# Kernel tuning notes

Hardware: AMD Instinct MI355X
Metric: run time of the kernel (lower is better)

## Reference

```python
import jax, jax.numpy as jnp
import numpy as np

B = 32           # graphs in batch
N_PER = 512      # nodes per graph
N = B * N_PER    # 16384 total nodes (block-diagonal batched graph)
E = N * 16       # 262144 edges
D_IN = 128
D_OUT = 128
ASSIGN = 2048    # total clusters = B * K
K = ASSIGN // B  # 64 clusters per graph


def setup_inputs() -> dict:
    key = jax.random.key(0)
    ks = jax.random.split(key, 6)
    h = jax.random.normal(ks[0], (N, D_IN), jnp.float32)
    # edges confined within each graph -> block-diagonal batched adjacency
    gid = jnp.repeat(jnp.arange(B), E // B)
    edge_src = (jax.random.randint(ks[1], (E,), 0, N_PER) + gid * N_PER).astype(jnp.int32)
    edge_dst = (jax.random.randint(ks[2], (E,), 0, N_PER) + gid * N_PER).astype(jnp.int32)
    # GraphSage NodeApply linears: Linear(2*in, out)
    stdv_f = 1.0 / np.sqrt(2 * D_IN)
    W_feat = jax.random.uniform(ks[3], (2 * D_IN, D_OUT), jnp.float32, -stdv_f, stdv_f)
    b_feat = jnp.zeros((D_OUT,), jnp.float32)
    W_pool = jax.random.uniform(ks[4], (2 * D_IN, ASSIGN), jnp.float32, -stdv_f, stdv_f)
    b_pool = jnp.zeros((ASSIGN,), jnp.float32)
    return {"h": h, "W_feat": W_feat, "b_feat": b_feat,
            "W_pool": W_pool, "b_pool": b_pool,
            "edge_src": edge_src, "edge_dst": edge_dst}


def _graphsage(h, W, b, src, dst):
    # mean aggregation over in-neighbors (dropout=0, batch_norm off)
    msg = jax.ops.segment_sum(h[src], dst, num_segments=N)          # [N, d_in]
    deg = jax.ops.segment_sum(jnp.ones((src.shape[0],), h.dtype), dst, num_segments=N)
    h_neigh = msg / jnp.maximum(deg, 1.0)[:, None]
    bundle = jnp.concatenate([h, h_neigh], axis=1) @ W + b          # [N, d_out]
    # F.normalize(p=2, dim=1) then activation, as in GraphSage NodeApply
    norm = jnp.linalg.norm(bundle, axis=1, keepdims=True)
    bundle = bundle / jnp.maximum(norm, 1e-12)
    return jax.nn.relu(bundle)


def _forward(h, W_feat, b_feat, W_pool, b_pool, src, dst):
    feat = _graphsage(h, W_feat, b_feat, src, dst)       # [N, D_OUT]
    assign = _graphsage(h, W_pool, b_pool, src, dst)     # [N, ASSIGN]
    # block-diagonal mask: node i of graph g may only assign to g's K clusters
    gid_n = jnp.arange(N) // N_PER                       # [N]
    gid_c = jnp.arange(ASSIGN) // K                      # [ASSIGN]
    mask = (gid_n[:, None] == gid_c[None, :]).astype(jnp.float32)
    # masked_softmax with memory_efficient=False
    s = jax.nn.softmax(assign * mask, axis=-1) * mask
    s = s / (s.sum(axis=-1, keepdims=True) + 1e-13)      # [N, ASSIGN]
    h_new = s.T @ feat                                   # [ASSIGN, D_OUT]
    # adj_new = S^T A S without densifying A: (A S)[dst] += S[src]
    a_s = jax.ops.segment_sum(s[src], dst, num_segments=N)
    adj_new = s.T @ a_s                                  # [ASSIGN, ASSIGN]
    return adj_new, h_new


def reference(h, W_feat, b_feat, W_pool, b_pool, edge_src, edge_dst):
    return _forward(h, W_feat, b_feat, W_pool, b_pool, edge_src, edge_dst)
```

## Files before the change

### kernel.cpp

```cpp
#include <hip/hip_runtime.h>

#define NB   32
#define NPER 512
#define NN   16384
#define EE   262144
#define DD   128
#define AS   2048
#define KC   64

using short8   = __attribute__((ext_vector_type(8))) short;
using floatx4  = __attribute__((ext_vector_type(4))) float;
using ushort4v = __attribute__((ext_vector_type(4))) unsigned short;

typedef __attribute__((address_space(3))) unsigned int lds_u32;
typedef const __attribute__((address_space(1))) unsigned int gbl_u32;

static __device__ __forceinline__ void gload16(const unsigned short* g, unsigned short* l) {
    __builtin_amdgcn_global_load_lds((gbl_u32*)g, (lds_u32*)l, 16, 0, 0);
}

static __device__ __forceinline__ float bits2f(unsigned int u) {
    union { unsigned int i; float f; } z; z.i = u << 16; return z.f;
}
static __device__ __forceinline__ unsigned short f2b(float x) {
    union { float f; unsigned int u; } v; v.f = x;
    unsigned int r = v.u + 0x7fffu + ((v.u >> 16) & 1u);
    return (unsigned short)(r >> 16);
}

union PrepSMem {
    unsigned short fT[128 * 136];
    float tl[32][33];
};
__global__ void prep_kernel(const float* __restrict__ h, unsigned short* __restrict__ bundle,
                            unsigned short* __restrict__ hT, const int* __restrict__ esrc,
                            const int* __restrict__ edst, unsigned int* __restrict__ Acnt,
                            const float* __restrict__ Wf, const float* __restrict__ Wp,
                            unsigned short* __restrict__ WfT, unsigned short* __restrict__ WpT) {
    __shared__ PrepSMem sm;
    int b = blockIdx.x, t = threadIdx.x;
    if (b < 128) {
        int node0 = b * 128;
        int r = t >> 1, hf = t & 1;
        const float4* h4 = reinterpret_cast<const float4*>(h + (size_t)(node0 + r) * 128 + hf * 64);
        unsigned short* bo = bundle + (size_t)(node0 + r) * 256 + hf * 64;
#pragma unroll
        for (int i = 0; i < 16; i++) {
            float4 v = h4[i];
            ushort4v o = { f2b(v.x), f2b(v.y), f2b(v.z), f2b(v.w) };
            *reinterpret_cast<ushort4v*>(bo + 4 * i) = o;
            int c = hf * 64 + 4 * i;
            sm.fT[(c + 0) * 136 + r] = o.x;
            sm.fT[(c + 1) * 136 + r] = o.y;
            sm.fT[(c + 2) * 136 + r] = o.z;
            sm.fT[(c + 3) * 136 + r] = o.w;
        }
        __syncthreads();
        int c = t >> 1, nh = t & 1;
        const uint4* src = reinterpret_cast<const uint4*>(&sm.fT[c * 136 + nh * 64]);
        uint4* dst = reinterpret_cast<uint4*>(hT + (size_t)c * NN + node0 + nh * 64);
#pragma unroll
        for (int i = 0; i < 8; i++) dst[i] = src[i];
    } else if (b < 1152) {
        int e = (b - 128) * 256 + t;
        int d = edst[e], sl = esrc[e] & 511;
        int idx = d * 512 + sl;
        atomicAdd(&Acnt[idx >> 2], 1u << (8 * (idx & 3)));
    } else {
        int tb = b - 1152;
        int bx = tb % 68, by = tb / 68;
        int tx = t & 31, ty = t >> 5;
        const float* in; unsigned short* out; int C, cb;
        if (bx < DD / 32) { in = Wf; out = WfT; C = DD; cb = bx; }
        else              { in = Wp; out = WpT; C = AS; cb = bx - DD / 32; }
        int c0 = cb * 32, r0 = by * 32;
        for (int i = 0; i < 4; i++)
            sm.tl[ty + 8 * i][tx] = in[(size_t)(r0 + ty + 8 * i) * C + c0 + tx];
        __syncthreads();
        for (int i = 0; i < 4; i++)
            out[(size_t)(c0 + ty + 8 * i) * 256 + r0 + tx] = f2b(sm.tl[tx][ty + 8 * i]);
    }
}

__global__ void conv_kernel(const unsigned int* __restrict__ Acnt,
                            unsigned short* __restrict__ Aadj, float* __restrict__ invdeg) {
    int t = threadIdx.x;
    int row = blockIdx.x * 8 + (t >> 5);
    int u = t & 31;
    uint4 w = reinterpret_cast<const uint4*>(Acnt)[(size_t)row * 32 + u];
    unsigned int wa[4] = { w.x, w.y, w.z, w.w };
    unsigned short out[16];
    float sum = 0.f;
#pragma unroll
    for (int i = 0; i < 4; i++) {
#pragma unroll
        for (int bb = 0; bb < 4; bb++) {
            float fv = (float)((wa[i] >> (8 * bb)) & 0xffu);
            sum += fv;
            out[4 * i + bb] = f2b(fv);
        }
    }
    unsigned int pw[8];
#pragma unroll
    for (int i = 0; i < 8; i++)
        pw[i] = (unsigned int)out[2 * i] | ((unsigned int)out[2 * i + 1] << 16);
    uint4* dst = reinterpret_cast<uint4*>(Aadj + (size_t)row * 512 + u * 16);
    uint4 s0 = { pw[0], pw[1], pw[2], pw[3] }, s1 = { pw[4], pw[5], pw[6], pw[7] };
    dst[0] = s0; dst[1] = s1;
#pragma unroll
    for (int d = 1; d < 32; d <<= 1) sum += __shfl_xor(sum, d, 64);
    if (u == 0) invdeg[row] = 1.0f / fmaxf(sum, 1.0f);
}

__global__ __launch_bounds__(256) void agg_h_mfma_kernel(
    const unsigned short* __restrict__ Aadj, const unsigned short* __restrict__ hT,
    const float* __restrict__ invdeg, unsigned short* __restrict__ bundle) {
    __shared__ alignas(16) unsigned short lA[64 * 512];
    int tid = threadIdx.x, bx = blockIdx.x;
    int r0 = bx * 64, g = bx >> 3;
    int wv = tid >> 6, lane = tid & 63, q = lane >> 4, lm = lane & 15;
    int mw = wv >> 1, nw = wv & 1;
#pragma unroll
    for (int j = 0; j < 16; j++) {
        int u = tid + 256 * j;
        int row = u >> 6, cu = (u & 63) ^ (row & 7);
        gload16(Aadj + (size_t)(r0 + row) * 512 + cu * 8, &lA[u * 8]);
    }
    floatx4 acc[2][4];
#pragma unroll
    for (int mt = 0; mt < 2; mt++)
#pragma unroll
        for (int nt = 0; nt < 4; nt++) acc[mt][nt] = (floatx4)0.f;
    __syncthreads();
    const unsigned short* Bb = hT + (size_t)(64 * nw + lm) * NN + g * 512 + (q << 3);
    short8 bF[2][4];
#pragma unroll
    for (int nt = 0; nt < 4; nt++)
        bF[0][nt] = *reinterpret_cast<const short8*>(Bb + (size_t)16 * nt * NN);
    for (int ki = 0; ki < 16; ki++) {
        if (ki < 15) {
#pragma unroll
            for (int nt = 0; nt < 4; nt++)
                bF[(ki + 1) & 1][nt] =
                    *reinterpret_cast<const short8*>(Bb + (size_t)16 * nt * NN + (ki + 1) * 32);
        }
        short8 aF[2];
        int swz = (4 * ki + q) ^ (lm & 7);
#pragma unroll
        for (int mt = 0; mt < 2; mt++)
            aF[mt] = *reinterpret_cast<const short8*>(&lA[((32 * mw + 16 * mt + lm) * 64 + swz) * 8]);
#pragma unroll
        for (int mt = 0; mt < 2; mt++)
#pragma unroll
            for (int nt = 0; nt < 4; nt++)
                acc[mt][nt] = __builtin_amdgcn_mfma_f32_16x16x32_bf16(aF[mt], bF[ki & 1][nt],
                                                                      acc[mt][nt], 0, 0, 0);
    }
#pragma unroll
    for (int mt = 0; mt < 2; mt++)
#pragma unroll
        for (int r = 0; r < 4; r++) {
            int row = 32 * mw + 16 * mt + 4 * q + r;
            float inv = invdeg[r0 + row];
#pragma unroll
            for (int nt = 0; nt < 4; nt++)
                bundle[(size_t)(r0 + row) * 256 + 128 + 64 * nw + 16 * nt + lm] =
                    f2b(acc[mt][nt][r] * inv);
        }
}

union FPSMem {
    struct { unsigned short lA[4096]; unsigned short lB[4096]; float red[256];
             unsigned short fT[17408]; } feat;
    struct { unsigned short lA[16384]; float raw[4352]; float ssq[256]; float rn[64]; } pool;
};
__global__ __launch_bounds__(256) void featpool_kernel(
    const unsigned short* __restrict__ bundle, const unsigned short* __restrict__ WfT,
    const unsigned short* __restrict__ WpT, const float* __restrict__ bfe,
    const float* __restrict__ bp, unsigned short* __restrict__ featT,
    unsigned short* __restrict__ sT) {
    __shared__ FPSMem sm;
    int tid = threadIdx.x, b = blockIdx.x;
    if (b < 128) {
        int r0 = b * 128;
        int wv = tid >> 6, lane = tid & 63;
        int mw = wv >> 1, nw = wv & 1, q = lane >> 4, lm = lane & 15;
        int rowS0 = tid >> 2,         cS0 = (tid & 3) ^ ((rowS0 >> 1) & 3);
        int rowS1 = (tid + 256) >> 2, cS1 = ((tid + 256) & 3) ^ ((rowS1 >> 1) & 3);
        int swz = q ^ ((lm >> 1) & 3);
        floatx4 acc[4][4];
#pragma unroll
        for (int mi = 0; mi < 4; mi++)
#pragma unroll
            for (int ni = 0; ni < 4; ni++) acc[mi][ni] = (floatx4)0.f;
        for (int k0 = 0; k0 < 256; k0 += 32) {
            gload16(bundle + (size_t)(r0 + rowS0) * 256 + k0 + 8 * cS0, &sm.feat.lA[tid * 8]);
            gload16(bundle + (size_t)(r0 + rowS1) * 256 + k0 + 8 * cS1, &sm.feat.lA[(tid + 256) * 8]);
            gload16(WfT + (size_t)rowS0 * 256 + k0 + 8 * cS0, &sm.feat.lB[tid * 8]);
            gload16(WfT + (size_t)rowS1 * 256 + k0 + 8 * cS1, &sm.feat.lB[(tid + 256) * 8]);
            __syncthreads();
            short8 aF[4], bF[4];
#pragma unroll
            for (int mi = 0; mi < 4; mi++)
                aF[mi] = *reinterpret_cast<const short8*>(&sm.feat.lA[((64 * mw + 16 * mi + lm) * 4 + swz) * 8]);
#pragma unroll
            for (int ni = 0; ni < 4; ni++)
                bF[ni] = *reinterpret_cast<const short8*>(&sm.feat.lB[((64 * nw + 16 * ni + lm) * 4 + swz) * 8]);
#pragma unroll
            for (int mi = 0; mi < 4; mi++)
#pragma unroll
                for (int ni = 0; ni < 4; ni++)
                    acc[mi][ni] = __builtin_amdgcn_mfma_f32_16x16x32_bf16(aF[mi], bF[ni], acc[mi][ni], 0, 0, 0);
            __syncthreads();
        }
#pragma unroll
        for (int ni = 0; ni < 4; ni++) {
            float bv = bfe[64 * nw + 16 * ni + lm];
#pragma unroll
            for (int mi = 0; mi < 4; mi++)
#pragma unroll
                for (int r = 0; r < 4; r++) acc[mi][ni][r] += bv;
        }
#pragma unroll
        for (int mi = 0; mi < 4; mi++)
#pragma unroll
            for (int r = 0; r < 4; r++) {
                float p = 0.f;
#pragma unroll
                for (int ni = 0; ni < 4; ni++) p += acc[mi][ni][r] * acc[mi][ni][r];
                p += __shfl_xor(p, 1, 64);
                p += __shfl_xor(p, 2, 64);
                p += __shfl_xor(p, 4, 64);
                p += __shfl_xor(p, 8, 64);
                if (lm == 0) sm.feat.red[nw * 128 + 64 * mw + 16 * mi + 4 * q + r] = p;
            }
        __syncthreads();
#pragma unroll
        for (int mi = 0; mi < 4; mi++) {
            float rrn[4];
#pragma unroll
            for (int r = 0; r < 4; r++) {
                int rl = 64 * mw + 16 * mi + 4 * q + r;
                rrn[r] = 1.0f / fmaxf(sqrtf(sm.feat.red[rl] + sm.feat.red[128 + rl]), 1e-12f);
            }
#pragma unroll
            for (int ni = 0; ni < 4; ni++) {
                int col = 64 * nw + 16 * ni + lm;
                ushort4v pk = { f2b(fmaxf(acc[mi][ni][0] * rrn[0], 0.f)),
                                f2b(fmaxf(acc[mi][ni][1] * rrn[1], 0.f)),
                                f2b(fmaxf(acc[mi][ni][2] * rrn[2], 0.f)),
                                f2b(fmaxf(acc[mi][ni][3] * rrn[3], 0.f)) };
                *reinterpret_cast<ushort4v*>(&sm.feat.fT[col * 136 + 64 * mw + 16 * mi + 4 * q]) = pk;
            }
        }
        __syncthreads();
        {
            int col = tid >> 1, half = tid & 1;
            const uint4* src = reinterpret_cast<const uint4*>(&sm.feat.fT[col * 136 + half * 64]);
            uint4* dst = reinterpret_cast<uint4*>(featT + (size_t)col * NN + r0 + half * 64);
#pragma unroll
            for (int i = 0; i < 8; i++) dst[i] = src[i];
        }
    } else {
        int bx = b - 128;
        int r0 = bx * 64, g = bx >> 3;
        int wv = tid >> 6, lane = tid & 63, q = lane >> 4, lm = lane & 15;
#pragma unroll
        for (int j = 0; j < 8; j++) {
            int u = tid + 256 * j;
            int row = u >> 5;
            int chunk = (u & 31) ^ (row & 7);
            gload16(bundle + (size_t)(r0 + row) * 256 + chunk * 8, &sm.pool.lA[u * 8]);
        }
        float ssqacc[4][4];
#pragma unroll
        for (int mi = 0; mi < 4; mi++)
#pragma unroll
            for (int r = 0; r < 4; r++) ssqacc[mi][r] = 0.f;
        __syncthreads();
        for (int nc8 = 0; nc8 < 8; nc8++) {
            int nc = 4 * nc8 + wv;
            const unsigned short* Bb = WpT + ((size_t)(nc * 64 + lm) << 8) + (q << 3);
            short8 bF[2][4];
#pragma unroll
            for (int ni = 0; ni < 4; ni++)
                bF[0][ni] = *reinterpret_cast<const short8*>(Bb + (ni << 12));
            floatx4 acc[4][4];
#pragma unroll
            for (int mi = 0; mi < 4; mi++)
#pragma unroll
                for (int ni = 0; ni < 4; ni++) acc[mi][ni] = (floatx4)0.f;
#pragma unroll
            for (int k = 0; k < 8; k++) {
                if (k < 7) {
#pragma unroll
                    for (int ni = 0; ni < 4; ni++)
                        bF[(k + 1) & 1][ni] =
                            *reinterpret_cast<const short8*>(Bb + (ni << 12) + ((k + 1) << 5));
                }
                short8 aF[4];
                int swz = (4 * k + q) ^ (lm & 7);
#pragma unroll
                for (int mi = 0; mi < 4; mi++)
                    aF[mi] = *reinterpret_cast<const short8*>(&sm.pool.lA[((16 * mi + lm) * 32 + swz) * 8]);
#pragma unroll
                for (int mi = 0; mi < 4; mi++)
#pragma unroll
                    for (int ni = 0; ni < 4; ni++)
                        acc[mi][ni] = __builtin_amdgcn_mfma_f32_16x16x32_bf16(aF[mi], bF[k & 1][ni],
                                                                              acc[mi][ni], 0, 0, 0);
            }
            float bv[4];
#pragma unroll
            for (int ni = 0; ni < 4; ni++) bv[ni] = bp[nc * 64 + 16 * ni + lm];
#pragma unroll
            for (int mi = 0; mi < 4; mi++)
#pragma unroll
                for (int r = 0; r < 4; r++) {
                    float p = 0.f;
#pragma unroll
                    for (int ni = 0; ni < 4; ni++) {
                        acc[mi][ni][r] += bv[ni];
                        p += acc[mi][ni][r] * acc[mi][ni][r];
                    }
                    ssqacc[mi][r] += p;
                }
            if (nc == g) {
#pragma unroll
                for (int mi = 0; mi < 4; mi++)
#pragma unroll
                    for (int ni = 0; ni < 4; ni++)
#pragma unroll
                        for (int r = 0; r < 4; r++)
                            sm.pool.raw[(16 * mi + 4 * q + r) * 68 + 16 * ni + lm] = acc[mi][ni][r];
            }
        }
#pragma unroll
        for (int mi = 0; mi < 4; mi++)
#pragma unroll
            for (int r = 0; r < 4; r++) {
                float p = ssqacc[mi][r];
                p += __shfl_xor(p, 1, 64);
                p += __shfl_xor(p, 2, 64);
                p += __shfl_xor(p, 4, 64);
                p += __shfl_xor(p, 8, 64);
                if (lm == 0) sm.pool.ssq[wv * 64 + 16 * mi + 4 * q + r] = p;
            }
        __syncthreads();
        if (tid < 64)
            sm.pool.rn[tid] = 1.0f / fmaxf(sqrtf(sm.pool.ssq[tid] + sm.pool.ssq[64 + tid] +
                                           sm.pool.ssq[128 + tid] + sm.pool.ssq[192 + tid]), 1e-12f);
        __syncthreads();
        {
            int row = tid >> 2, j = tid & 3;
            int nloc = ((bx & 7) << 6) + row;
            float rn = sm.pool.rn[row];
            float v[16];
            float mx = -1e30f;
#pragma unroll
            for (int c4 = 0; c4 < 4; c4++) {
                float4 rv = *reinterpret_cast<const float4*>(&sm.pool.raw[row * 68 + 16 * j + 4 * c4]);
                v[4 * c4 + 0] = fmaxf(rv.x * rn, 0.f);
                v[4 * c4 + 1] = fmaxf(rv.y * rn, 0.f);
                v[4 * c4 + 2] = fmaxf(rv.z * rn, 0.f);
                v[4 * c4 + 3] = fmaxf(rv.w * rn, 0.f);
            }
#pragma unroll
            for (int c = 0; c < 16; c++) mx = fmaxf(mx, v[c]);
            mx = fmaxf(mx, __shfl_xor(mx, 1, 64));
            mx = fmaxf(mx, __shfl_xor(mx, 2, 64));
            float z = 0.f;
#pragma unroll
            for (int c = 0; c < 16; c++) { v[c] = __expf(v[c] - mx); z += v[c]; }
            z += __shfl_xor(z, 1, 64);
            z += __shfl_xor(z, 2, 64);
            float iz = 1.0f / z;
#pragma unroll
            for (int c4 = 0; c4 < 4; c4++) {
                size_t tb = (size_t)(g * KC + 16 * j + 4 * c4) * NPER + nloc;
                sT[tb] = f2b(v[4 * c4 + 0] * iz);
                sT[tb + NPER] = f2b(v[4 * c4 + 1] * iz);
                sT[tb + 2 * NPER] = f2b(v[4 * c4 + 2] * iz);
                sT[tb + 3 * NPER] = f2b(v[4 * c4 + 3] * iz);
            }
        }
    }
}

__global__ __launch_bounds__(256) void as_mfma_kernel(
    const unsigned short* __restrict__ sT, const unsigned short* __restrict__ Aadj,
    unsigned short* __restrict__ asT) {
    __shared__ alignas(16) unsigned short lS[64 * 512];
    int tid = threadIdx.x, bx = blockIdx.x;
    int g = bx >> 1, half = bx & 1;
    int wv = tid >> 6, lane = tid & 63, q = lane >> 4, lm = lane & 15;
#pragma unroll
    for (int j = 0; j < 16; j++) {
        int u = tid + 256 * j;
        int row = u >> 6, cu = (u & 63) ^ (row & 7);
        gload16(sT + (size_t)(g * KC + row) * NPER + cu * 8, &lS[u * 8]);
    }
    floatx4 acc[4][4];
#pragma unroll
    for (int mi = 0; mi < 4; mi++)
#pragma unroll
        for (int nt = 0; nt < 4; nt++) acc[mi][nt] = (floatx4)0.f;
    __syncthreads();
    int dbase = half * 256 + wv * 64;
    const unsigned short* Bb = Aadj + (size_t)(g * 512 + dbase + lm) * 512 + (q << 3);
    short8 bF[2][4];
#pragma unroll
    for (int nt = 0; nt < 4; nt++)
        bF[0][nt] = *reinterpret_cast<const short8*>(Bb + (size_t)16 * nt * 512);
    for (int ki = 0; ki < 16; ki++) {
        if (ki < 15) {
#pragma unroll
            for (int nt = 0; nt < 4; nt++)
                bF[(ki + 1) & 1][nt] =
                    *reinterpret_cast<const short8*>(Bb + (size_t)16 * nt * 512 + (ki + 1) * 32);
        }
        short8 aF[4];
        int swz = (4 * ki + q) ^ (lm & 7);
#pragma unroll
        for (int mi = 0; mi < 4; mi++)
            aF[mi] = *reinterpret_cast<const short8*>(&lS[((16 * mi + lm) * 64 + swz) * 8]);
#pragma unroll
        for (int mi = 0; mi < 4; mi++)
#pragma unroll
            for (int nt = 0; nt < 4; nt++)
                acc[mi][nt] = __builtin_amdgcn_mfma_f32_16x16x32_bf16(aF[mi], bF[ki & 1][nt],
                                                                      acc[mi][nt], 0, 0, 0);
    }
#pragma unroll
    for (int mi = 0; mi < 4; mi++)
#pragma unroll
        for (int r = 0; r < 4; r++) {
            int row = 16 * mi + 4 * q + r;
#pragma unroll
            for (int nt = 0; nt < 4; nt++)
                asT[(size_t)(g * KC + row) * NPER + dbase + 16 * nt + lm] = f2b(acc[mi][nt][r]);
        }
}

__global__ __launch_bounds__(256) void hnew_adj2_kernel(
    const unsigned short* __restrict__ sT, const unsigned short* __restrict__ featT,
    const unsigned short* __restrict__ asT, float* __restrict__ adjf,
    float* __restrict__ hnewf) {
    __shared__ alignas(16) unsigned short lS[1024 * 8];
    __shared__ alignas(16) unsigned short lF[2048 * 8];
    __shared__ alignas(16) unsigned short lAS[1024 * 8];
    int tid = threadIdx.x, b = blockIdx.x;
    if (b >= 32) {
        uint4 z = { 0u, 0u, 0u, 0u };
        for (int row = b - 32; row < AS; row += 224) {
            int g = row >> 6;
            uint4* out = reinterpret_cast<uint4*>(adjf + (size_t)row * AS);
            for (int i = tid; i < 512; i += 256)
                if (i < g * 16 || i >= g * 16 + 16) out[i] = z;
        }
        return;
    }
    int g = b;
    int wv = tid >> 6, lane = tid & 63, q = lane >> 4, lm = lane & 15;
    bool isH = (wv < 2);
    floatx4 accH[4][4];
    floatx4 accA[4][2];
#pragma unroll
    for (int mi = 0; mi < 4; mi++) {
#pragma unroll
        for (int ni = 0; ni < 4; ni++) accH[mi][ni] = (floatx4)0.f;
#pragma unroll
        for (int ni = 0; ni < 2; ni++) accA[mi][ni] = (floatx4)0.f;
    }
    for (int ks = 0; ks < 4; ks++) {
#pragma unroll
        for (int j = 0; j < 4; j++) {
            int u = tid + 256 * j;
            int row = u >> 4, cu = (u & 15) ^ (row & 15);
            gload16(sT + (size_t)(g * KC + row) * NPER + ks * 128 + cu * 8, &lS[u * 8]);
        }
#pragma unroll
        for (int j = 0; j < 8; j++) {
            int u = tid + 256 * j;
            int row = u >> 4, cu = (u & 15) ^ (row & 15);
            gload16(featT + (size_t)row * NN + g * NPER + ks * 128 + cu * 8, &lF[u * 8]);
        }
#pragma unroll
        for (int j = 0; j < 4; j++) {
            int u = tid + 256 * j;
            int row = u >> 4, cu = (u & 15) ^ (row & 15);
            gload16(asT + (size_t)(g * KC + row) * NPER + ks * 128 + cu * 8, &lAS[u * 8]);
        }
        __syncthreads();
#pragma unroll
        for (int kk = 0; kk < 4; kk++) {
            short8 aF[4];
#pragma unroll
            for (int mi = 0; mi < 4; mi++)
                aF[mi] = *reinterpret_cast<const short8*>(
                    &lS[((16 * mi + lm) * 16 + ((4 * kk + q) ^ lm)) * 8]);
            if (isH) {
                short8 bF[4];
#pragma unroll
                for (int ni = 0; ni < 4; ni++)
                    bF[ni] = *reinterpret_cast<const short8*>(
                        &lF[((64 * wv + 16 * ni + lm) * 16 + ((4 * kk + q) ^ lm)) * 8]);
#pragma unroll
                for (int mi = 0; mi < 4; mi++)
#pragma unroll
                    for (int ni = 0; ni < 4; ni++)
                        accH[mi][ni] = __builtin_amdgcn_mfma_f32_16x16x32_bf16(aF[mi], bF[ni],
                                                                               accH[mi][ni], 0, 0, 0);
            } else {
                short8 bF[2];
#pragma unroll
                for (int ni = 0; ni < 2; ni++)
                    bF[ni] = *reinterpret_cast<const short8*>(
                        &lAS[((32 * (wv - 2) + 16 * ni + lm) * 16 + ((4 * kk + q) ^ lm)) * 8]);
#pragma unroll
                for (int mi = 0; mi < 4; mi++)
#pragma unroll
                    for (int ni = 0; ni < 2; ni++)
                        accA[mi][ni] = __builtin_amdgcn_mfma_f32_16x16x32_bf16(aF[mi], bF[ni],
                                                                               accA[mi][ni], 0, 0, 0);
            }
        }
        __syncthreads();
    }
    if (isH) {
#pragma unroll
        for (int mi = 0; mi < 4; mi++)
#pragma unroll
            for (int ni = 0; ni < 4; ni++)
#pragma unroll
                for (int r = 0; r < 4; r++)
                    hnewf[(size_t)(g * KC + 16 * mi + 4 * q + r) * DD +
                          64 * wv + 16 * ni + lm] = accH[mi][ni][r];
    } else {
#pragma unroll
        for (int mi = 0; mi < 4; mi++)
#pragma unroll
            for (int ni = 0; ni < 2; ni++)
#pragma unroll
                for (int r = 0; r < 4; r++)
                    adjf[(size_t)(g * KC + 16 * mi + 4 * q + r) * AS +
                         g * KC + 32 * (wv - 2) + 16 * ni + lm] = accA[mi][ni][r];
    }
}

extern "C" void kernel_launch(void* const* d_in, const int* in_sizes, int n_in,
                              void* d_out, int out_size, void* d_ws, size_t ws_size,
                              hipStream_t stream) {
    const float* h   = (const float*)d_in[0];
    const float* Wf  = (const float*)d_in[1];
    const float* bfe = (const float*)d_in[2];
    const float* Wp  = (const float*)d_in[3];
    const float* bp  = (const float*)d_in[4];
    const int* esrc  = (const int*)d_in[5];
    const int* edst  = (const int*)d_in[6];

    float* adjf  = (float*)d_out;
    float* hnewf = adjf + (size_t)AS * AS;

    unsigned short* bundle = (unsigned short*)d_ws;
    unsigned short* WfT   = bundle + (size_t)NN * 256;
    unsigned short* WpT   = WfT + 128 * 256;
    unsigned short* sT    = WpT + (size_t)AS * 256;
    unsigned short* asT   = sT + (size_t)NN * KC;
    unsigned short* featT = asT + (size_t)NN * KC;
    unsigned short* hT    = featT + (size_t)DD * NN;
    unsigned short* Aadj  = hT + (size_t)DD * NN;
    float* invdeg = (float*)(Aadj + (size_t)NN * 512);
    unsigned int* Acnt = (unsigned int*)(invdeg + NN);

    hipMemsetAsync(Acnt, 0, (size_t)NN * 512, stream);

    prep_kernel<<<128 + EE / 256 + 544, 256, 0, stream>>>(h, bundle, hT, esrc, edst, Acnt,
                                                          Wf, Wp, WfT, WpT);
    conv_kernel<<<NN / 8, 256, 0, stream>>>(Acnt, Aadj, invdeg);
    agg_h_mfma_kernel<<<NN / 64, 256, 0, stream>>>(Aadj, hT, invdeg, bundle);
    featpool_kernel<<<384, 256, 0, stream>>>(bundle, WfT, WpT, bfe, bp, featT, sT);
    as_mfma_kernel<<<NB * 2, 256, 0, stream>>>(sT, Aadj, asT);
    hnew_adj2_kernel<<<256, 256, 0, stream>>>(sT, featT, asT, adjf, hnewf);
}
```

Measured before the change: 181.2 us.

## Compute pool-row norms via Gram matrix of W_pool instead of full 2048-wide GEMM

```diff
diff --git a/kernel.cpp b/kernel.cpp
--- a/kernel.cpp
+++ b/kernel.cpp
@@ -36,7 +36,8 @@
                             unsigned short* __restrict__ hT, const int* __restrict__ esrc,
                             const int* __restrict__ edst, unsigned int* __restrict__ Acnt,
                             const float* __restrict__ Wf, const float* __restrict__ Wp,
-                            unsigned short* __restrict__ WfT, unsigned short* __restrict__ WpT) {
+                            unsigned short* __restrict__ WfT, unsigned short* __restrict__ WpT,
+                            unsigned short* __restrict__ Wpb) {
     __shared__ PrepSMem sm;
     int b = blockIdx.x, t = threadIdx.x;
     if (b < 128) {
@@ -66,7 +67,7 @@
         int d = edst[e], sl = esrc[e] & 511;
         int idx = d * 512 + sl;
         atomicAdd(&Acnt[idx >> 2], 1u << (8 * (idx & 3)));
-    } else {
+    } else if (b < 1696) {
         int tb = b - 1152;
         int bx = tb % 68, by = tb / 68;
         int tx = t & 31, ty = t >> 5;
@@ -79,44 +80,127 @@
         __syncthreads();
         for (int i = 0; i < 4; i++)
             out[(size_t)(c0 + ty + 8 * i) * 256 + r0 + tx] = f2b(sm.tl[tx][ty + 8 * i]);
-    }
-}
-
-__global__ void conv_kernel(const unsigned int* __restrict__ Acnt,
-                            unsigned short* __restrict__ Aadj, float* __restrict__ invdeg) {
-    int t = threadIdx.x;
-    int row = blockIdx.x * 8 + (t >> 5);
-    int u = t & 31;
-    uint4 w = reinterpret_cast<const uint4*>(Acnt)[(size_t)row * 32 + u];
-    unsigned int wa[4] = { w.x, w.y, w.z, w.w };
-    unsigned short out[16];
-    float sum = 0.f;
-#pragma unroll
-    for (int i = 0; i < 4; i++) {
-#pragma unroll
-        for (int bb = 0; bb < 4; bb++) {
-            float fv = (float)((wa[i] >> (8 * bb)) & 0xffu);
-            sum += fv;
-            out[4 * i + bb] = f2b(fv);
-        }
-    }
-    unsigned int pw[8];
-#pragma unroll
-    for (int i = 0; i < 8; i++)
-        pw[i] = (unsigned int)out[2 * i] | ((unsigned int)out[2 * i + 1] << 16);
-    uint4* dst = reinterpret_cast<uint4*>(Aadj + (size_t)row * 512 + u * 16);
-    uint4 s0 = { pw[0], pw[1], pw[2], pw[3] }, s1 = { pw[4], pw[5], pw[6], pw[7] };
-    dst[0] = s0; dst[1] = s1;
-#pragma unroll
-    for (int d = 1; d < 32; d <<= 1) sum += __shfl_xor(sum, d, 64);
-    if (u == 0) invdeg[row] = 1.0f / fmaxf(sum, 1.0f);
+    } else {
+        int gid = (b - 1696) * 256 + t;
+        float4 v = reinterpret_cast<const float4*>(Wp)[gid];
+        ushort4v o = { f2b(v.x), f2b(v.y), f2b(v.z), f2b(v.w) };
+        *reinterpret_cast<ushort4v*>(&Wpb[(size_t)gid * 4]) = o;
+    }
+}
+
+__global__ __launch_bounds__(256) void conv_kernel(
+    const unsigned int* __restrict__ Acnt, unsigned short* __restrict__ Aadj,
+    float* __restrict__ invdeg, const unsigned short* __restrict__ Wpb,
+    const float* __restrict__ Wp, const float* __restrict__ bp,
+    float* __restrict__ Gf, float* __restrict__ uF, float* __restrict__ cF) {
+    __shared__ alignas(16) unsigned short glA[4096];
+    __shared__ alignas(16) unsigned short glB[4096];
+    __shared__ float gcred[4];
+    int t = threadIdx.x, b = blockIdx.x;
+    if (b < 2048) {
+        int row = b * 8 + (t >> 5);
+        int u = t & 31;
+        uint4 w = reinterpret_cast<const uint4*>(Acnt)[(size_t)row * 32 + u];
+        unsigned int wa[4] = { w.x, w.y, w.z, w.w };
+        unsigned short out[16];
+        float sum = 0.f;
+#pragma unroll
+        for (int i = 0; i < 4; i++) {
+#pragma unroll
+            for (int bb = 0; bb < 4; bb++) {
+                float fv = (float)((wa[i] >> (8 * bb)) & 0xffu);
+                sum += fv;
+                out[4 * i + bb] = f2b(fv);
+            }
+        }
+        unsigned int pw[8];
+#pragma unroll
+        for (int i = 0; i < 8; i++)
+            pw[i] = (unsigned int)out[2 * i] | ((unsigned int)out[2 * i + 1] << 16);
+        uint4* dst = reinterpret_cast<uint4*>(Aadj + (size_t)row * 512 + u * 16);
+        uint4 s0 = { pw[0], pw[1], pw[2], pw[3] }, s1 = { pw[4], pw[5], pw[6], pw[7] };
+        dst[0] = s0; dst[1] = s1;
+#pragma unroll
+        for (int d = 1; d < 32; d <<= 1) sum += __shfl_xor(sum, d, 64);
+        if (u == 0) invdeg[row] = 1.0f / fmaxf(sum, 1.0f);
+        return;
+    }
+    int b2 = b - 2048;
+    int ks = b2 >> 2, ti = (b2 >> 1) & 1, tj = b2 & 1;
+    int wv = t >> 6, lane = t & 63;
+    int mw = wv >> 1, nw = wv & 1, q = lane >> 4, lm = lane & 15;
+    int rowS0 = t >> 2,         cS0 = (t & 3) ^ ((rowS0 >> 1) & 3);
+    int rowS1 = (t + 256) >> 2, cS1 = ((t + 256) & 3) ^ ((rowS1 >> 1) & 3);
+    int swz = q ^ ((lm >> 1) & 3);
+    floatx4 acc[4][4];
+#pragma unroll
+    for (int mi = 0; mi < 4; mi++)
+#pragma unroll
+        for (int ni = 0; ni < 4; ni++) acc[mi][ni] = (floatx4)0.f;
+    for (int ki = 0; ki < 16; ki++) {
+        int k0 = ks * 512 + ki * 32;
+        gload16(Wpb + (size_t)(ti * 128 + rowS0) * 2048 + k0 + 8 * cS0, &glA[t * 8]);
+        gload16(Wpb + (size_t)(ti * 128 + rowS1) * 2048 + k0 + 8 * cS1, &glA[(t + 256) * 8]);
+        gload16(Wpb + (size_t)(tj * 128 + rowS0) * 2048 + k0 + 8 * cS0, &glB[t * 8]);
+        gload16(Wpb + (size_t)(tj * 128 + rowS1) * 2048 + k0 + 8 * cS1, &glB[(t + 256) * 8]);
+        __syncthreads();
+        short8 aF[4], bF[4];
+#pragma unroll
+        for (int mi = 0; mi < 4; mi++)
+            aF[mi] = *reinterpret_cast<const short8*>(&glA[((64 * mw + 16 * mi + lm) * 4 + swz) * 8]);
+#pragma unroll
+        for (int ni = 0; ni < 4; ni++)
+            bF[ni] = *reinterpret_cast<const short8*>(&glB[((64 * nw + 16 * ni + lm) * 4 + swz) * 8]);
+#pragma unroll
+        for (int mi = 0; mi < 4; mi++)
+#pragma unroll
+            for (int ni = 0; ni < 4; ni++)
+                acc[mi][ni] = __builtin_amdgcn_mfma_f32_16x16x32_bf16(aF[mi], bF[ni], acc[mi][ni], 0, 0, 0);
+        __syncthreads();
+    }
+#pragma unroll
+    for (int mi = 0; mi < 4; mi++)
+#pragma unroll
+        for (int ni = 0; ni < 4; ni++)
+#pragma unroll
+            for (int r = 0; r < 4; r++)
+                atomicAdd(&Gf[(size_t)(ti * 128 + 64 * mw + 16 * mi + 4 * q + r) * 256 +
+                              tj * 128 + 64 * nw + 16 * ni + lm], acc[mi][ni][r]);
+    if (tj == 0) {
+        int row = t >> 1, jh = t & 1;
+        const float* wr = Wp + (size_t)(ti * 128 + row) * 2048 + ks * 512 + jh * 256;
+        const float* br = bp + ks * 512 + jh * 256;
+        float s = 0.f;
+        for (int j = 0; j < 256; j++) s += wr[j] * br[j];
+        atomicAdd(&uF[ti * 128 + row], s);
+    }
+    if (b2 == 0) {
+        float s = 0.f;
+        for (int j = t; j < 2048; j += 256) { float v = bp[j]; s += v * v; }
+#pragma unroll
+        for (int d = 1; d < 64; d <<= 1) s += __shfl_xor(s, d, 64);
+        if (lane == 0) gcred[wv] = s;
+        __syncthreads();
+        if (t == 0) atomicAdd(cF, gcred[0] + gcred[1] + gcred[2] + gcred[3]);
+    }
 }
 
 __global__ __launch_bounds__(256) void agg_h_mfma_kernel(
     const unsigned short* __restrict__ Aadj, const unsigned short* __restrict__ hT,
-    const float* __restrict__ invdeg, unsigned short* __restrict__ bundle) {
+    const float* __restrict__ invdeg, unsigned short* __restrict__ bundle,
+    const float* __restrict__ Gf, unsigned short* __restrict__ Gb) {
     __shared__ alignas(16) unsigned short lA[64 * 512];
     int tid = threadIdx.x, bx = blockIdx.x;
+    if (bx >= 256) {
+        int base = (bx - 256) * 16384;
+        for (int i = 0; i < 16; i++) {
+            int idx = base + i * 1024 + tid * 4;
+            float4 v = *reinterpret_cast<const float4*>(Gf + idx);
+            ushort4v o = { f2b(v.x), f2b(v.y), f2b(v.z), f2b(v.w) };
+            *reinterpret_cast<ushort4v*>(&Gb[idx]) = o;
+        }
+        return;
+    }
     int r0 = bx * 64, g = bx >> 3;
     int wv = tid >> 6, lane = tid & 63, q = lane >> 4, lm = lane & 15;
     int mw = wv >> 1, nw = wv & 1;
@@ -171,14 +255,16 @@
 
 union FPSMem {
     struct { unsigned short lA[4096]; unsigned short lB[4096]; float red[256];
-             unsigned short fT[17408]; } feat;
-    struct { unsigned short lA[16384]; float raw[4352]; float ssq[256]; float rn[64]; } pool;
+             unsigned short fT2[8704]; } feat;
+    struct { unsigned short lA[16384]; float raw[4352]; float ssq[256]; float rn[64];
+             float uL[256]; } pool;
 };
 __global__ __launch_bounds__(256) void featpool_kernel(
     const unsigned short* __restrict__ bundle, const unsigned short* __restrict__ WfT,
-    const unsigned short* __restrict__ WpT, const float* __restrict__ bfe,
-    const float* __restrict__ bp, unsigned short* __restrict__ featT,
-    unsigned short* __restrict__ sT) {
+    const unsigned short* __restrict__ WpT, const unsigned short* __restrict__ Gb,
+    const float* __restrict__ bfe, const float* __restrict__ bp,
+    const float* __restrict__ uF, const float* __restrict__ cF,
+    unsigned short* __restrict__ featT, unsigned short* __restrict__ sT) {
     __shared__ FPSMem sm;
     int tid = threadIdx.x, b = blockIdx.x;
     if (b < 128) {
@@ -235,31 +321,36 @@
                 if (lm == 0) sm.feat.red[nw * 128 + 64 * mw + 16 * mi + 4 * q + r] = p;
             }
         __syncthreads();
-#pragma unroll
-        for (int mi = 0; mi < 4; mi++) {
-            float rrn[4];
-#pragma unroll
-            for (int r = 0; r < 4; r++) {
-                int rl = 64 * mw + 16 * mi + 4 * q + r;
-                rrn[r] = 1.0f / fmaxf(sqrtf(sm.feat.red[rl] + sm.feat.red[128 + rl]), 1e-12f);
-            }
-#pragma unroll
-            for (int ni = 0; ni < 4; ni++) {
-                int col = 64 * nw + 16 * ni + lm;
-                ushort4v pk = { f2b(fmaxf(acc[mi][ni][0] * rrn[0], 0.f)),
-                                f2b(fmaxf(acc[mi][ni][1] * rrn[1], 0.f)),
-                                f2b(fmaxf(acc[mi][ni][2] * rrn[2], 0.f)),
-                                f2b(fmaxf(acc[mi][ni][3] * rrn[3], 0.f)) };
-                *reinterpret_cast<ushort4v*>(&sm.feat.fT[col * 136 + 64 * mw + 16 * mi + 4 * q]) = pk;
-            }
-        }
-        __syncthreads();
-        {
-            int col = tid >> 1, half = tid & 1;
-            const uint4* src = reinterpret_cast<const uint4*>(&sm.feat.fT[col * 136 + half * 64]);
-            uint4* dst = reinterpret_cast<uint4*>(featT + (size_t)col * NN + r0 + half * 64);
-#pragma unroll
-            for (int i = 0; i < 8; i++) dst[i] = src[i];
+        for (int rd = 0; rd < 2; rd++) {
+            if (nw == rd) {
+#pragma unroll
+                for (int mi = 0; mi < 4; mi++) {
+                    float rrn[4];
+#pragma unroll
+                    for (int r = 0; r < 4; r++) {
+                        int rl = 64 * mw + 16 * mi + 4 * q + r;
+                        rrn[r] = 1.0f / fmaxf(sqrtf(sm.feat.red[rl] + sm.feat.red[128 + rl]), 1e-12f);
+                    }
+#pragma unroll
+                    for (int ni = 0; ni < 4; ni++) {
+                        int col_loc = 16 * ni + lm;
+                        ushort4v pk = { f2b(fmaxf(acc[mi][ni][0] * rrn[0], 0.f)),
+                                        f2b(fmaxf(acc[mi][ni][1] * rrn[1], 0.f)),
+                                        f2b(fmaxf(acc[mi][ni][2] * rrn[2], 0.f)),
+                                        f2b(fmaxf(acc[mi][ni][3] * rrn[3], 0.f)) };
+                        *reinterpret_cast<ushort4v*>(&sm.feat.fT2[col_loc * 136 + 64 * mw + 16 * mi + 4 * q]) = pk;
+                    }
+                }
+            }
+            __syncthreads();
+#pragma unroll
+            for (int i = 0; i < 4; i++) {
+                int idx = tid + 256 * i;
+                int cl = idx >> 4, pos = idx & 15;
+                uint4 v = *reinterpret_cast<const uint4*>(&sm.feat.fT2[cl * 136 + pos * 8]);
+                *reinterpret_cast<uint4*>(featT + (size_t)(64 * rd + cl) * NN + r0 + pos * 8) = v;
+            }
+            __syncthreads();
         }
     } else {
         int bx = b - 128;
@@ -272,15 +363,10 @@
             int chunk = (u & 31) ^ (row & 7);
             gload16(bundle + (size_t)(r0 + row) * 256 + chunk * 8, &sm.pool.lA[u * 8]);
         }
-        float ssqacc[4][4];
-#pragma unroll
-        for (int mi = 0; mi < 4; mi++)
-#pragma unroll
-            for (int r = 0; r < 4; r++) ssqacc[mi][r] = 0.f;
-        __syncthreads();
-        for (int nc8 = 0; nc8 < 8; nc8++) {
-            int nc = 4 * nc8 + wv;
-            const unsigned short* Bb = WpT + ((size_t)(nc * 64 + lm) << 8) + (q << 3);
+        sm.pool.uL[tid] = uF[tid];
+        __syncthreads();
+        {
+            const unsigned short* Bb = Gb + ((size_t)(wv * 64 + lm) << 8) + (q << 3);
             short8 bF[2][4];
 #pragma unroll
             for (int ni = 0; ni < 4; ni++)
@@ -310,46 +396,59 @@
                         acc[mi][ni] = __builtin_amdgcn_mfma_f32_16x16x32_bf16(aF[mi], bF[k & 1][ni],
                                                                               acc[mi][ni], 0, 0, 0);
             }
-            float bv[4];
-#pragma unroll
-            for (int ni = 0; ni < 4; ni++) bv[ni] = bp[nc * 64 + 16 * ni + lm];
+            float uc[4];
+#pragma unroll
+            for (int ni = 0; ni < 4; ni++) uc[ni] = sm.pool.uL[64 * wv + 16 * ni + lm];
 #pragma unroll
             for (int mi = 0; mi < 4; mi++)
 #pragma unroll
                 for (int r = 0; r < 4; r++) {
+                    int row = 16 * mi + 4 * q + r;
                     float p = 0.f;
 #pragma unroll
                     for (int ni = 0; ni < 4; ni++) {
-                        acc[mi][ni][r] += bv[ni];
-                        p += acc[mi][ni][r] * acc[mi][ni][r];
+                        int col = 64 * wv + 16 * ni + lm;
+                        int cu = (col >> 3) ^ (row & 7);
+                        float xv = bits2f((unsigned int)sm.pool.lA[(row * 32 + cu) * 8 + (col & 7)]);
+                        p += (acc[mi][ni][r] + 2.f * uc[ni]) * xv;
                     }
-                    ssqacc[mi][r] += p;
+                    p += __shfl_xor(p, 1, 64);
+                    p += __shfl_xor(p, 2, 64);
+                    p += __shfl_xor(p, 4, 64);
+                    p += __shfl_xor(p, 8, 64);
+                    if (lm == 0) sm.pool.ssq[wv * 64 + row] = p;
                 }
-            if (nc == g) {
+        }
+        {
+            const unsigned short* Bb2 = WpT + (size_t)(g * KC + 16 * wv + lm) * 256 + (q << 3);
+            short8 b2[2];
+            b2[0] = *reinterpret_cast<const short8*>(Bb2);
+            floatx4 acc2[4];
+#pragma unroll
+            for (int mi = 0; mi < 4; mi++) acc2[mi] = (floatx4)0.f;
+#pragma unroll
+            for (int k = 0; k < 8; k++) {
+                if (k < 7) b2[(k + 1) & 1] = *reinterpret_cast<const short8*>(Bb2 + ((k + 1) << 5));
+                short8 aF[4];
+                int swz = (4 * k + q) ^ (lm & 7);
 #pragma unroll
                 for (int mi = 0; mi < 4; mi++)
-#pragma unroll
-                    for (int ni = 0; ni < 4; ni++)
-#pragma unroll
-                        for (int r = 0; r < 4; r++)
-                            sm.pool.raw[(16 * mi + 4 * q + r) * 68 + 16 * ni + lm] = acc[mi][ni][r];
-            }
-        }
-#pragma unroll
-        for (int mi = 0; mi < 4; mi++)
-#pragma unroll
-            for (int r = 0; r < 4; r++) {
-                float p = ssqacc[mi][r];
-                p += __shfl_xor(p, 1, 64);
-                p += __shfl_xor(p, 2, 64);
-                p += __shfl_xor(p, 4, 64);
-                p += __shfl_xor(p, 8, 64);
-                if (lm == 0) sm.pool.ssq[wv * 64 + 16 * mi + 4 * q + r] = p;
-            }
+                    aF[mi] = *reinterpret_cast<const short8*>(&sm.pool.lA[((16 * mi + lm) * 32 + swz) * 8]);
+#pragma unroll
+                for (int mi = 0; mi < 4; mi++)
+                    acc2[mi] = __builtin_amdgcn_mfma_f32_16x16x32_bf16(aF[mi], b2[k & 1], acc2[mi], 0, 0, 0);
+            }
+            float bv = bp[g * KC + 16 * wv + lm];
+#pragma unroll
+            for (int mi = 0; mi < 4; mi++)
+#pragma unroll
+                for (int r = 0; r < 4; r++)
+                    sm.pool.raw[(16 * mi + 4 * q + r) * 68 + 16 * wv + lm] = acc2[mi][r] + bv;
+        }
         __syncthreads();
         if (tid < 64)
             sm.pool.rn[tid] = 1.0f / fmaxf(sqrtf(sm.pool.ssq[tid] + sm.pool.ssq[64 + tid] +
-                                           sm.pool.ssq[128 + tid] + sm.pool.ssq[192 + tid]), 1e-12f);
+                                           sm.pool.ssq[128 + tid] + sm.pool.ssq[192 + tid] + cF[0]), 1e-12f);
         __syncthreads();
         {
             int row = tid >> 2, j = tid & 3;
@@ -572,14 +671,18 @@
     unsigned short* Aadj  = hT + (size_t)DD * NN;
     float* invdeg = (float*)(Aadj + (size_t)NN * 512);
     unsigned int* Acnt = (unsigned int*)(invdeg + NN);
-
-    hipMemsetAsync(Acnt, 0, (size_t)NN * 512, stream);
-
-    prep_kernel<<<128 + EE / 256 + 544, 256, 0, stream>>>(h, bundle, hT, esrc, edst, Acnt,
-                                                          Wf, Wp, WfT, WpT);
-    conv_kernel<<<NN / 8, 256, 0, stream>>>(Acnt, Aadj, invdeg);
-    agg_h_mfma_kernel<<<NN / 64, 256, 0, stream>>>(Aadj, hT, invdeg, bundle);
-    featpool_kernel<<<384, 256, 0, stream>>>(bundle, WfT, WpT, bfe, bp, featT, sT);
+    float* Gf = (float*)(Acnt + (size_t)NN * 128);
+    float* uF = Gf + 65536;
+    float* cF = uF + 256;
+    unsigned short* Wpb = (unsigned short*)(cF + 4);
+    unsigned short* Gb  = Wpb + (size_t)256 * 2048;
+
+    hipMemsetAsync(Acnt, 0, (size_t)NN * 512 + (65536 + 256 + 4) * sizeof(float), stream);
+
+    prep_kernel<<<2208, 256, 0, stream>>>(h, bundle, hT, esrc, edst, Acnt, Wf, Wp, WfT, WpT, Wpb);
+    conv_kernel<<<2064, 256, 0, stream>>>(Acnt, Aadj, invdeg, Wpb, Wp, bp, Gf, uF, cF);
+    agg_h_mfma_kernel<<<260, 256, 0, stream>>>(Aadj, hT, invdeg, bundle, Gf, Gb);
+    featpool_kernel<<<384, 256, 0, stream>>>(bundle, WfT, WpT, Gb, bfe, bp, uF, cF, featT, sT);
     as_mfma_kernel<<<NB * 2, 256, 0, stream>>>(sT, Aadj, asT);
     hnew_adj2_kernel<<<256, 256, 0, stream>>>(sT, featT, asT, adjf, hnewf);
 }
```

Result: faster. 174.1 us (-3.9%).
